# Kernel tuning notes

Hardware: AMD Instinct MI355X
Metric: run time of the kernel (lower is better)

## Reference

```python
import jax, jax.numpy as jnp
import numpy as np

HIDDEN = 1024
N_HEADS = 16
HEAD_DIM = HIDDEN // N_HEADS
WINDOW = 256  # symmetric window: keys j with i - W//2 <= j <= i + W//2
BATCH, SEQ = 2, 2048


def setup_inputs() -> dict:
    key = jax.random.key(0)
    ks = jax.random.split(key, 9)
    s = 0.02
    return {
        "x":  jax.random.normal(ks[0], (BATCH, SEQ, HIDDEN), dtype=jnp.float32),
        "wq": jax.random.normal(ks[1], (HIDDEN, HIDDEN), dtype=jnp.float32) * s,
        "bq": jnp.zeros((HIDDEN,), dtype=jnp.float32),
        "wk": jax.random.normal(ks[2], (HIDDEN, HIDDEN), dtype=jnp.float32) * s,
        "bk": jnp.zeros((HIDDEN,), dtype=jnp.float32),
        "wv": jax.random.normal(ks[3], (HIDDEN, HIDDEN), dtype=jnp.float32) * s,
        "bv": jnp.zeros((HIDDEN,), dtype=jnp.float32),
        "wo": jax.random.normal(ks[4], (HIDDEN, HIDDEN), dtype=jnp.float32) * s,
        "bo": jnp.zeros((HIDDEN,), dtype=jnp.float32),
    }


def reference(x, wq, bq, wk, bk, wv, bv, wo, bo):
    B, S, Hs = x.shape
    scale = HEAD_DIM ** -0.5

    def proj(w, b):
        # [B,S,Hs] -> [B,H,S,D]
        return (x @ w + b).reshape(B, S, N_HEADS, HEAD_DIM).transpose(0, 2, 1, 3)

    q = proj(wq, bq)
    k = proj(wk, bk)
    v = proj(wv, bv)

    # Clipped sliding window == band-masked full attention (identical softmax weights).
    scores = jnp.einsum('bhid,bhjd->bhij', q, k) * scale  # [B,H,S,S]
    i = jnp.arange(S)[:, None]
    j = jnp.arange(S)[None, :]
    band = (j >= i - WINDOW // 2) & (j <= i + WINDOW // 2)
    scores = jnp.where(band, scores, -jnp.inf)
    attn = jax.nn.softmax(scores, axis=-1)
    out = jnp.einsum('bhij,bhjd->bhid', attn, v)  # [B,H,S,D]
    out = out.transpose(0, 2, 1, 3).reshape(B, S, Hs)
    return out @ wo + bo
```

## Files before the change

### kernel.cpp

```cpp
#include <hip/hip_runtime.h>
#include <hip/hip_bf16.h>
#include <stdint.h>

#define BATCH 2
#define SEQ   2048
#define HID   1024
#define NH    16
#define HD    64
#define W2    128

using bhalf8 = __attribute__((ext_vector_type(8))) short;
using fvec4  = __attribute__((ext_vector_type(4))) float;
using u16x8  = __attribute__((ext_vector_type(8))) unsigned short;

__device__ __forceinline__ unsigned short f2bf(float f) {
    union { float f; unsigned int u; } c; c.f = f;
    unsigned int u = c.u;
    u += 0x7FFFu + ((u >> 16) & 1u);
    return (unsigned short)(u >> 16);
}

__device__ __forceinline__ fvec4 zero4() {
    fvec4 z = {0.f, 0.f, 0.f, 0.f};
    return z;
}

__device__ __forceinline__ void load_lds16(const void* g, void* l) {
    __builtin_amdgcn_global_load_lds(
        (const __attribute__((address_space(1))) void*)g,
        (__attribute__((address_space(3))) void*)l, 16, 0, 0);
}

__device__ __forceinline__ float rowmax16(float v) {
    v = fmaxf(v, __shfl_xor(v, 1));
    v = fmaxf(v, __shfl_xor(v, 2));
    v = fmaxf(v, __shfl_xor(v, 4));
    v = fmaxf(v, __shfl_xor(v, 8));
    return v;
}
__device__ __forceinline__ float rowsum16(float v) {
    v += __shfl_xor(v, 1);
    v += __shfl_xor(v, 2);
    v += __shfl_xor(v, 4);
    v += __shfl_xor(v, 8);
    return v;
}


__global__ __launch_bounds__(256) void k_convert_x(const float* __restrict__ x,
                                                   unsigned short* __restrict__ xb) {
    int i = (blockIdx.x * 256 + threadIdx.x) * 8;
    float4 a = *(const float4*)(x + i);
    float4 b = *(const float4*)(x + i + 4);
    u16x8 o;
    o[0] = f2bf(a.x); o[1] = f2bf(a.y); o[2] = f2bf(a.z); o[3] = f2bf(a.w);
    o[4] = f2bf(b.x); o[5] = f2bf(b.y); o[6] = f2bf(b.z); o[7] = f2bf(b.w);
    *(u16x8*)(xb + i) = o;
}

__global__ __launch_bounds__(256) void k_transpose_w(
    const float* __restrict__ w0, const float* __restrict__ w1,
    const float* __restrict__ w2, const float* __restrict__ w3,
    unsigned short* __restrict__ t0, unsigned short* __restrict__ t1,
    unsigned short* __restrict__ t2, unsigned short* __restrict__ t3) {
    int z = blockIdx.z;
    const float* src = (z == 0) ? w0 : (z == 1) ? w1 : (z == 2) ? w2 : w3;
    unsigned short* dst = (z == 0) ? t0 : (z == 1) ? t1 : (z == 2) ? t2 : t3;
    __shared__ float tile[32][33];
    int n0 = blockIdx.x * 32, k0 = blockIdx.y * 32;
    int tx = threadIdx.x, ty = threadIdx.y;
#pragma unroll
    for (int r = 0; r < 4; ++r)
        tile[ty + 8 * r][tx] = src[(size_t)(k0 + ty + 8 * r) * HID + n0 + tx];
    __syncthreads();
#pragma unroll
    for (int r = 0; r < 4; ++r)
        dst[(size_t)(n0 + ty + 8 * r) * HID + k0 + tx] = f2bf(tile[tx][ty + 8 * r]);
}


__device__ __forceinline__ void stage_tile(const unsigned short* __restrict__ A,
                                           const unsigned short* __restrict__ Bt,
                                           int m0, int n0, int k0,
                                           unsigned short* As, unsigned short* Bs,
                                           int t) {
    int row = t >> 2, ch = t & 3;
    int chs = ch ^ ((row >> 1) & 3);
    load_lds16(A + (size_t)(m0 + row) * HID + k0 + chs * 8, As + t * 8);
    load_lds16(Bt + (size_t)(n0 + row) * HID + k0 + chs * 8, Bs + t * 8);
}

__device__ __forceinline__ void gemm_tile8(const unsigned short* __restrict__ A,
                                           const unsigned short* __restrict__ Bt,
                                           int m0, int n0,
                                           unsigned short* As, unsigned short* Bs,
                                           fvec4 acc[4][2]) {
    const int t = threadIdx.x;
    const int lane = t & 63;
    const int wid = t >> 6;
    const int wr = wid >> 2, wc = wid & 3;
    const int c16 = lane & 15, g = lane >> 4;

#pragma unroll
    for (int mi = 0; mi < 4; ++mi)
#pragma unroll
        for (int ni = 0; ni < 2; ++ni) acc[mi][ni] = zero4();

    stage_tile(A, Bt, m0, n0, 0, As, Bs, t);
    stage_tile(A, Bt, m0, n0, 32, As + 4096, Bs + 4096, t);

    int cur = 0, sb = 2;
    for (int k0 = 0; k0 < HID; k0 += 32) {
        if (k0 + 32 < HID)
            asm volatile("s_waitcnt vmcnt(2)" ::: "memory");
        else
            asm volatile("s_waitcnt vmcnt(0)" ::: "memory");
        asm volatile("s_waitcnt lgkmcnt(0)" ::: "memory");
        __builtin_amdgcn_sched_barrier(0);
        __builtin_amdgcn_s_barrier();

        if (k0 + 64 < HID) {
            stage_tile(A, Bt, m0, n0, k0 + 64, As + sb * 4096, Bs + sb * 4096, t);
            sb = (sb == 2) ? 0 : sb + 1;
        }

        const unsigned short* Ab = As + cur * 4096;
        const unsigned short* Bb = Bs + cur * 4096;
        bhalf8 af[4], bf[2];
#pragma unroll
        for (int i = 0; i < 4; ++i) {
            int ra = wr * 64 + i * 16 + c16;
            af[i] = *(const bhalf8*)(Ab + ra * 32 + (g ^ ((ra >> 1) & 3)) * 8);
        }
#pragma unroll
        for (int i = 0; i < 2; ++i) {
            int rb = wc * 32 + i * 16 + c16;
            bf[i] = *(const bhalf8*)(Bb + rb * 32 + (g ^ ((rb >> 1) & 3)) * 8);
        }
#pragma unroll
        for (int mi = 0; mi < 4; ++mi)
#pragma unroll
            for (int ni = 0; ni < 2; ++ni)
                acc[mi][ni] = __builtin_amdgcn_mfma_f32_16x16x32_bf16(
                    af[mi], bf[ni], acc[mi][ni], 0, 0, 0);
        cur = (cur == 2) ? 0 : cur + 1;
    }
}

__global__ __launch_bounds__(512, 6) void k_gemm_qkv(
    const unsigned short* __restrict__ xb,
    const unsigned short* __restrict__ wqt, const unsigned short* __restrict__ wkt,
    const unsigned short* __restrict__ wvt,
    const float* __restrict__ bq, const float* __restrict__ bk, const float* __restrict__ bv,
    unsigned short* __restrict__ qb, unsigned short* __restrict__ kbuf,
    unsigned short* __restrict__ vt) {
    __shared__ unsigned short SH[2][3 * 128 * 32];
    const int z = blockIdx.z;
    const unsigned short* Bt = (z == 0) ? wqt : (z == 1) ? wkt : wvt;
    const float* bias = (z == 0) ? bq : (z == 1) ? bk : bv;
    const int m0 = blockIdx.y * 128, n0 = blockIdx.x * 128;
    fvec4 acc[4][2];
    gemm_tile8(xb, Bt, m0, n0, SH[0], SH[1], acc);

    const int t = threadIdx.x, lane = t & 63, wid = t >> 6;
    const int wr = wid >> 2, wc = wid & 3, c16 = lane & 15, g = lane >> 4;

    if (z != 2) {
#pragma unroll
        for (int mi = 0; mi < 4; ++mi) {
#pragma unroll
            for (int ni = 0; ni < 2; ++ni) {
                int gcol = n0 + wc * 32 + ni * 16 + c16;
                int h = gcol >> 6, d = gcol & 63;
                float bsv = bias[gcol];
#pragma unroll
                for (int r = 0; r < 4; ++r) {
                    int grow = m0 + wr * 64 + mi * 16 + 4 * g + r;
                    int b = grow >> 11, s = grow & (SEQ - 1);
                    float v = acc[mi][ni][r] + bsv;
                    if (z == 0)
                        qb[((size_t)(b * NH + h) * SEQ + s) * HD + d] = f2bf(v * 0.125f);
                    else
                        kbuf[((size_t)(b * NH + h) * SEQ + s) * HD + d] = f2bf(v);
                }
            }
        }
    } else {
        unsigned short* VL = &SH[0][0];
        __syncthreads();
#pragma unroll
        for (int mi = 0; mi < 4; ++mi)
#pragma unroll
            for (int ni = 0; ni < 2; ++ni) {
                int dl = wc * 32 + ni * 16 + c16;
                float bsv = bias[n0 + dl];
#pragma unroll
                for (int r = 0; r < 4; ++r) {
                    int sl = wr * 64 + mi * 16 + 4 * g + r;
                    VL[dl * 132 + sl] = f2bf(acc[mi][ni][r] + bsv);
                }
            }
        __syncthreads();
        const int b = m0 >> 11, sbase = m0 & (SEQ - 1);
#pragma unroll
        for (int it = 0; it < 4; ++it) {
            int slot = t + 512 * it;
            int dl = slot >> 4, ch = slot & 15;
            int gcol = n0 + dl;
            int h = gcol >> 6, d = gcol & 63;
            u16x8 v = *(const u16x8*)(VL + dl * 132 + ch * 8);
            *(u16x8*)(vt + ((size_t)(b * NH + h) * HD + d) * SEQ + sbase + ch * 8) = v;
        }
    }
}

__global__ __launch_bounds__(512, 6) void k_gemm_out(
    const unsigned short* __restrict__ attn, const unsigned short* __restrict__ wot,
    const float* __restrict__ bo, float* __restrict__ out) {
    __shared__ unsigned short SH[2][3 * 128 * 32];
    const int m0 = blockIdx.y * 128, n0 = blockIdx.x * 128;
    fvec4 acc[4][2];
    gemm_tile8(attn, wot, m0, n0, SH[0], SH[1], acc);

    const int lane = threadIdx.x & 63, wid = threadIdx.x >> 6;
    const int wr = wid >> 2, wc = wid & 3, c16 = lane & 15, g = lane >> 4;
#pragma unroll
    for (int mi = 0; mi < 4; ++mi) {
#pragma unroll
        for (int ni = 0; ni < 2; ++ni) {
            int gcol = n0 + wc * 32 + ni * 16 + c16;
            float bsv = bo[gcol];
#pragma unroll
            for (int r = 0; r < 4; ++r) {
                int grow = m0 + wr * 64 + mi * 16 + 4 * g + r;
                out[(size_t)grow * HID + gcol] = acc[mi][ni][r] + bsv;
            }
        }
    }
}

__global__ __launch_bounds__(256) void k_attn(
    const unsigned short* __restrict__ qb, const unsigned short* __restrict__ kbuf,
    const unsigned short* __restrict__ vt, unsigned short* __restrict__ attn) {
    const int bh = blockIdx.y;
    const int wid = threadIdx.x >> 6, lane = threadIdx.x & 63;
    const int g = lane >> 4, c16 = lane & 15;
    const int q0 = blockIdx.x * 64 + wid * 16;

    const unsigned short* Qp = qb + (size_t)bh * SEQ * HD;
    const unsigned short* Kp = kbuf + (size_t)bh * SEQ * HD;
    const unsigned short* Vp = vt + (size_t)bh * HD * SEQ;

    __shared__ unsigned short Plds[4][16 * 32];
    unsigned short* myP = Plds[wid];

    bhalf8 qf0, qf1;
    {
        const unsigned short* p = Qp + (size_t)(q0 + c16) * HD + g * 8;
        qf0 = *(const bhalf8*)p;
        qf1 = *(const bhalf8*)(p + 32);
    }
    fvec4 acc[4];
#pragma unroll
    for (int i = 0; i < 4; ++i) acc[i] = zero4();
    float mrow[4] = {-1e30f, -1e30f, -1e30f, -1e30f};
    float srow[4] = {0.f, 0.f, 0.f, 0.f};

    int kstart = q0 - W2; if (kstart < 0) kstart = 0; kstart &= ~31;
    int kend = q0 + 15 + W2; if (kend > SEQ - 1) kend = SEQ - 1;

    for (int t0 = kstart; t0 <= kend; t0 += 32) {
        fvec4 sc0 = zero4(), sc1 = zero4();
        {
            const unsigned short* kp = Kp + (size_t)(t0 + c16) * HD + g * 8;
            bhalf8 ka = *(const bhalf8*)kp;
            bhalf8 kb2 = *(const bhalf8*)(kp + 32);
            sc0 = __builtin_amdgcn_mfma_f32_16x16x32_bf16(qf0, ka, sc0, 0, 0, 0);
            sc0 = __builtin_amdgcn_mfma_f32_16x16x32_bf16(qf1, kb2, sc0, 0, 0, 0);
        }
        {
            const unsigned short* kp = Kp + (size_t)(t0 + 16 + c16) * HD + g * 8;
            bhalf8 ka = *(const bhalf8*)kp;
            bhalf8 kb2 = *(const bhalf8*)(kp + 32);
            sc1 = __builtin_amdgcn_mfma_f32_16x16x32_bf16(qf0, ka, sc1, 0, 0, 0);
            sc1 = __builtin_amdgcn_mfma_f32_16x16x32_bf16(qf1, kb2, sc1, 0, 0, 0);
        }
#pragma unroll
        for (int r = 0; r < 4; ++r) {
            int ia = q0 + 4 * g + r;
            int j0 = t0 + c16, j1 = t0 + 16 + c16;
            if (j0 < ia - W2 || j0 > ia + W2) sc0[r] = -1e30f;
            if (j1 < ia - W2 || j1 > ia + W2) sc1[r] = -1e30f;
        }
#pragma unroll
        for (int r = 0; r < 4; ++r) {
            float pm = rowmax16(fmaxf(sc0[r], sc1[r]));
            float mn = fmaxf(mrow[r], pm);
            float f = __expf(mrow[r] - mn);
            mrow[r] = mn;
            float p0 = __expf(sc0[r] - mn);
            float p1 = __expf(sc1[r] - mn);
            srow[r] = srow[r] * f + (p0 + p1);
#pragma unroll
            for (int db = 0; db < 4; ++db) acc[db][r] *= f;
            myP[(4 * g + r) * 32 + c16] = f2bf(p0);
            myP[(4 * g + r) * 32 + 16 + c16] = f2bf(p1);
        }
        asm volatile("s_waitcnt lgkmcnt(0)" ::: "memory");
        __builtin_amdgcn_sched_barrier(0);
        bhalf8 pf = *(const bhalf8*)(myP + c16 * 32 + g * 8);
#pragma unroll
        for (int db = 0; db < 4; ++db) {
            const unsigned short* vp = Vp + (size_t)(db * 16 + c16) * SEQ + t0 + g * 8;
            bhalf8 vf = *(const bhalf8*)vp;
            acc[db] = __builtin_amdgcn_mfma_f32_16x16x32_bf16(pf, vf, acc[db], 0, 0, 0);
        }
    }

    float inv[4];
#pragma unroll
    for (int r = 0; r < 4; ++r) inv[r] = 1.f / rowsum16(srow[r]);

    const int b = bh >> 4, h = bh & 15;
#pragma unroll
    for (int db = 0; db < 4; ++db)
#pragma unroll
        for (int r = 0; r < 4; ++r) {
            int si = q0 + 4 * g + r;
            attn[((size_t)(b * SEQ) + si) * HID + h * HD + db * 16 + c16] =
                f2bf(acc[db][r] * inv[r]);
        }
}


extern "C" void kernel_launch(void* const* d_in, const int* in_sizes, int n_in,
                              void* d_out, int out_size, void* d_ws, size_t ws_size,
                              hipStream_t stream) {
    const float* x  = (const float*)d_in[0];
    const float* wq = (const float*)d_in[1];
    const float* bq = (const float*)d_in[2];
    const float* wk = (const float*)d_in[3];
    const float* bk = (const float*)d_in[4];
    const float* wv = (const float*)d_in[5];
    const float* bv = (const float*)d_in[6];
    const float* wo = (const float*)d_in[7];
    const float* bo = (const float*)d_in[8];
    float* out = (float*)d_out;

    char* ws = (char*)d_ws;
    unsigned short* xb   = (unsigned short*)(ws);
    unsigned short* wqt  = (unsigned short*)(ws + (8u << 20));
    unsigned short* wkt  = wqt + 1024 * 1024;
    unsigned short* wvt  = wkt + 1024 * 1024;
    unsigned short* wot  = wvt + 1024 * 1024;
    unsigned short* qb   = wot + 1024 * 1024;
    unsigned short* kbuf = qb + 4u * 1024 * 1024;
    unsigned short* vt   = kbuf + 4u * 1024 * 1024;
    unsigned short* attn = vt + 4u * 1024 * 1024;

    k_convert_x<<<dim3(2048), dim3(256), 0, stream>>>(x, xb);
    k_transpose_w<<<dim3(32, 32, 4), dim3(32, 8), 0, stream>>>(wq, wk, wv, wo,
                                                               wqt, wkt, wvt, wot);
    k_gemm_qkv<<<dim3(8, 32, 3), dim3(512), 0, stream>>>(xb, wqt, wkt, wvt,
                                                         bq, bk, bv, qb, kbuf, vt);
    k_attn<<<dim3(SEQ / 64, BATCH * NH), dim3(256), 0, stream>>>(qb, kbuf, vt, attn);
    k_gemm_out<<<dim3(8, 32), dim3(512), 0, stream>>>(attn, wot, bo, out);
}
```

Baseline: 181.2 us.

## Switch GEMM mainloop to K=64 double-buffered tiles with MFMA priority boost

New measurement: 180.4 us. About the same (-0.4%).

```diff
diff --git a/kernel.cpp b/kernel.cpp
--- a/kernel.cpp
+++ b/kernel.cpp
@@ -79,15 +79,19 @@
 }
 
 
-__device__ __forceinline__ void stage_tile(const unsigned short* __restrict__ A,
-                                           const unsigned short* __restrict__ Bt,
-                                           int m0, int n0, int k0,
-                                           unsigned short* As, unsigned short* Bs,
-                                           int t) {
-    int row = t >> 2, ch = t & 3;
-    int chs = ch ^ ((row >> 1) & 3);
-    load_lds16(A + (size_t)(m0 + row) * HID + k0 + chs * 8, As + t * 8);
-    load_lds16(Bt + (size_t)(n0 + row) * HID + k0 + chs * 8, Bs + t * 8);
+__device__ __forceinline__ void stage_tile64(const unsigned short* __restrict__ A,
+                                             const unsigned short* __restrict__ Bt,
+                                             int m0, int n0, int k0,
+                                             unsigned short* As, unsigned short* Bs,
+                                             int t) {
+#pragma unroll
+    for (int i = 0; i < 2; ++i) {
+        int chunk = t + 512 * i;
+        int row = chunk >> 3, ch = chunk & 7;
+        int chs = ch ^ (row & 7);
+        load_lds16(A + (size_t)(m0 + row) * HID + k0 + chs * 8, As + chunk * 8);
+        load_lds16(Bt + (size_t)(n0 + row) * HID + k0 + chs * 8, Bs + chunk * 8);
+    }
 }
 
 __device__ __forceinline__ void gemm_tile8(const unsigned short* __restrict__ A,
@@ -106,55 +110,56 @@
 #pragma unroll
         for (int ni = 0; ni < 2; ++ni) acc[mi][ni] = zero4();
 
-    stage_tile(A, Bt, m0, n0, 0, As, Bs, t);
-    stage_tile(A, Bt, m0, n0, 32, As + 4096, Bs + 4096, t);
-
-    int cur = 0, sb = 2;
-    for (int k0 = 0; k0 < HID; k0 += 32) {
-        if (k0 + 32 < HID)
-            asm volatile("s_waitcnt vmcnt(2)" ::: "memory");
-        else
-            asm volatile("s_waitcnt vmcnt(0)" ::: "memory");
-        asm volatile("s_waitcnt lgkmcnt(0)" ::: "memory");
+    stage_tile64(A, Bt, m0, n0, 0, As, Bs, t);
+
+    int cur = 0;
+    for (int k0 = 0; k0 < HID; k0 += 64) {
+        asm volatile("s_waitcnt vmcnt(0)" ::: "memory");
         __builtin_amdgcn_sched_barrier(0);
         __builtin_amdgcn_s_barrier();
 
-        if (k0 + 64 < HID) {
-            stage_tile(A, Bt, m0, n0, k0 + 64, As + sb * 4096, Bs + sb * 4096, t);
-            sb = (sb == 2) ? 0 : sb + 1;
-        }
-
-        const unsigned short* Ab = As + cur * 4096;
-        const unsigned short* Bb = Bs + cur * 4096;
-        bhalf8 af[4], bf[2];
-#pragma unroll
-        for (int i = 0; i < 4; ++i) {
-            int ra = wr * 64 + i * 16 + c16;
-            af[i] = *(const bhalf8*)(Ab + ra * 32 + (g ^ ((ra >> 1) & 3)) * 8);
-        }
-#pragma unroll
-        for (int i = 0; i < 2; ++i) {
-            int rb = wc * 32 + i * 16 + c16;
-            bf[i] = *(const bhalf8*)(Bb + rb * 32 + (g ^ ((rb >> 1) & 3)) * 8);
-        }
-#pragma unroll
-        for (int mi = 0; mi < 4; ++mi)
-#pragma unroll
-            for (int ni = 0; ni < 2; ++ni)
-                acc[mi][ni] = __builtin_amdgcn_mfma_f32_16x16x32_bf16(
-                    af[mi], bf[ni], acc[mi][ni], 0, 0, 0);
-        cur = (cur == 2) ? 0 : cur + 1;
-    }
-}
-
-__global__ __launch_bounds__(512, 6) void k_gemm_qkv(
+        if (k0 + 64 < HID)
+            stage_tile64(A, Bt, m0, n0, k0 + 64,
+                         As + (cur ^ 1) * 8192, Bs + (cur ^ 1) * 8192, t);
+
+        const unsigned short* Ab = As + cur * 8192;
+        const unsigned short* Bb = Bs + cur * 8192;
+        bhalf8 af[2][4], bf[2][2];
+#pragma unroll
+        for (int ks = 0; ks < 2; ++ks) {
+#pragma unroll
+            for (int i = 0; i < 4; ++i) {
+                int ra = wr * 64 + i * 16 + c16;
+                af[ks][i] = *(const bhalf8*)(Ab + ra * 64 + ((4 * ks + g) ^ (ra & 7)) * 8);
+            }
+#pragma unroll
+            for (int i = 0; i < 2; ++i) {
+                int rb = wc * 32 + i * 16 + c16;
+                bf[ks][i] = *(const bhalf8*)(Bb + rb * 64 + ((4 * ks + g) ^ (rb & 7)) * 8);
+            }
+        }
+        __builtin_amdgcn_s_setprio(1);
+#pragma unroll
+        for (int ks = 0; ks < 2; ++ks)
+#pragma unroll
+            for (int mi = 0; mi < 4; ++mi)
+#pragma unroll
+                for (int ni = 0; ni < 2; ++ni)
+                    acc[mi][ni] = __builtin_amdgcn_mfma_f32_16x16x32_bf16(
+                        af[ks][mi], bf[ks][ni], acc[mi][ni], 0, 0, 0);
+        __builtin_amdgcn_s_setprio(0);
+        cur ^= 1;
+    }
+}
+
+__global__ __launch_bounds__(512, 4) void k_gemm_qkv(
     const unsigned short* __restrict__ xb,
     const unsigned short* __restrict__ wqt, const unsigned short* __restrict__ wkt,
     const unsigned short* __restrict__ wvt,
     const float* __restrict__ bq, const float* __restrict__ bk, const float* __restrict__ bv,
     unsigned short* __restrict__ qb, unsigned short* __restrict__ kbuf,
     unsigned short* __restrict__ vt) {
-    __shared__ unsigned short SH[2][3 * 128 * 32];
+    __shared__ unsigned short SH[2][2 * 128 * 64];
     const int z = blockIdx.z;
     const unsigned short* Bt = (z == 0) ? wqt : (z == 1) ? wkt : wvt;
     const float* bias = (z == 0) ? bq : (z == 1) ? bk : bv;
@@ -214,10 +219,10 @@
     }
 }
 
-__global__ __launch_bounds__(512, 6) void k_gemm_out(
+__global__ __launch_bounds__(512, 4) void k_gemm_out(
     const unsigned short* __restrict__ attn, const unsigned short* __restrict__ wot,
     const float* __restrict__ bo, float* __restrict__ out) {
-    __shared__ unsigned short SH[2][3 * 128 * 32];
+    __shared__ unsigned short SH[2][2 * 128 * 64];
     const int m0 = blockIdx.y * 128, n0 = blockIdx.x * 128;
     fvec4 acc[4][2];
     gemm_tile8(attn, wot, m0, n0, SH[0], SH[1], acc);
```
